# Performance work log

Hardware: AMD Instinct MI355X
Metric: run time of the kernel (lower is better)

Reference implementation:

```python
import jax, jax.numpy as jnp
import numpy as np

N_HEADS, N_LEVELS, N_POINTS, D_MODEL = 8, 3, 12, 64
PARAM_NAMES = ['vp0_w','vp0_b','vp1_w','vp1_b','so0_w','so0_b','so1_w','so1_b','so2_w','so2_b','so3_w','so3_b','aw0_w','aw0_b','aw1_w','aw1_b','aw2_w','aw2_b','aw3_w','aw3_b','op0_w','op0_b','op1_w','op1_b']

def _lrelu(x):
    return jnp.where(x >= 0, x, 0.1 * x)

def _conv(x, w, b):
    y = jax.lax.conv_general_dilated(x, w, (1, 1), 'SAME', dimension_numbers=('NCHW', 'OIHW', 'NCHW'))
    return y + b[None, :, None, None]

def _bilinear(img, px, py):
    # img [B,C,H,W]; px,py [B,Q] absolute pixel coords; zero padding (grid_sample 'zeros')
    B, C, H, W = img.shape
    flat = img.reshape(B, C, H * W)
    x0 = jnp.floor(px); y0 = jnp.floor(py)
    wx1 = px - x0; wy1 = py - y0
    def g(xi, yi, wgt):
        valid = (xi >= 0) & (xi <= W - 1) & (yi >= 0) & (yi <= H - 1)
        xi_c = jnp.clip(xi, 0, W - 1).astype(jnp.int32)
        yi_c = jnp.clip(yi, 0, H - 1).astype(jnp.int32)
        v = jnp.take_along_axis(flat, (yi_c * W + xi_c)[:, None, :], axis=2)
        return v * (wgt * valid)[:, None, :]
    return (g(x0, y0, (1 - wx1) * (1 - wy1)) + g(x0 + 1, y0, wx1 * (1 - wy1))
          + g(x0, y0 + 1, (1 - wx1) * wy1) + g(x0 + 1, y0 + 1, wx1 * wy1))

def _flow_warp(img, flow):
    # img [n,C,h,w]; flow [n,2,h,w] (x,y); matches grid_sample align_corners=True
    n, C, h, w = img.shape
    gy, gx = jnp.meshgrid(jnp.arange(h, dtype=img.dtype), jnp.arange(w, dtype=img.dtype), indexing='ij')
    px = (gx[None] + flow[:, 0]).reshape(n, h * w)
    py = (gy[None] + flow[:, 1]).reshape(n, h * w)
    return _bilinear(img, px, py).reshape(n, C, h, w)

def _forward(x, flow_1, flow_2, flip_flow_1, flip_flow_2, p):
    n, t, c, h, w = x.shape
    hw = h * w; THW = t * hw
    M, L, P, D = N_HEADS, N_LEVELS, N_POINTS, c // N_HEADS
    flow_cn1 = flow_1
    flow_cn2 = flow_1 + _flow_warp(flow_2, flow_1)
    flow_n1c, flow_n1n2 = flip_flow_1, flow_2
    flow_n2n1 = flip_flow_2
    flow_n2c = flip_flow_2 + _flow_warp(flip_flow_1, flip_flow_2)
    warp_cn1 = _flow_warp(x[:, 1], flow_cn1)
    warp_cn2 = _flow_warp(x[:, 2], flow_cn2)
    warp_n1c = _flow_warp(x[:, 0], flow_n1c)
    warp_n1n2 = _flow_warp(x[:, 2], flow_n1n2)
    warp_n2n1 = _flow_warp(x[:, 1], flow_n2n1)
    warp_n2c = _flow_warp(x[:, 0], flow_n2c)
    extra = jnp.concatenate([x[:, 0], warp_cn1, warp_cn2, warp_n1c, warp_n1n2, warp_n2n1, warp_n2c,
                             flow_cn1, flow_cn2, flow_n1c, flow_n1n2, flow_n2n1, flow_n2c], axis=1)
    value = _conv(_lrelu(_conv(x.reshape(n, t * c, h, w), p['vp0_w'], p['vp0_b'])), p['vp1_w'], p['vp1_b'])
    def head(e, pre):
        y = _lrelu(_conv(e, p[pre + '0_w'], p[pre + '0_b']))
        y = _lrelu(_conv(y, p[pre + '1_w'], p[pre + '1_b']))
        y = _lrelu(_conv(y, p[pre + '2_w'], p[pre + '2_b']))
        return _conv(y, p[pre + '3_w'], p[pre + '3_b'])
    so = head(extra, 'so')  # [n, L*M*L*P*2, h, w]
    aw = head(extra, 'aw')  # [n, L*M*L*P*9, h, w]
    so = so.reshape(n, t, -1, hw).transpose(0, 1, 3, 2).reshape(n, THW, M, L, P, 2)
    aw = aw.reshape(n, t, -1, hw).transpose(0, 1, 3, 2).reshape(n, THW, M, L * P * 9)
    aw = jax.nn.softmax(aw, axis=-1).reshape(n, THW, M, L, P * 9)
    # flow-guided offsets: add per-(query-frame, target-level) flow to learned offsets
    off = so.reshape(n, t, hw, M, L, P, 2)
    fz = jnp.zeros_like(flow_cn2)
    def lvl(f0, f1, f2):
        s = jnp.stack([f0, f1, f2], 1)  # [n,3,2,h,w]
        return s.transpose(0, 3, 4, 1, 2).reshape(n, hw, L, 2)[:, None, :, None, :, None, :]
    off = jnp.concatenate([
        off[:, 0:1] + lvl(fz, flow_cn1, flow_cn2),
        off[:, 1:2] + lvl(flow_n1c, fz, flow_n1n2),
        off[:, 2:3] + lvl(flow_n2c, flow_n2n1, fz)], axis=1).reshape(n, THW, M, L, P, 2)
    # 3x3 integer patch around each sampling point
    pi, pj = jnp.meshgrid(jnp.arange(-1, 2), jnp.arange(-1, 2), indexing='ij')
    patch = jnp.stack([pi, pj], -1).reshape(1, 1, 1, 1, 1, 9, 2).astype(off.dtype)
    off = (off[..., None, :] + patch).reshape(n, THW, M, L, P * 9, 2)
    # reference points (valid_ratios are all 1: full masks are zeros)
    ry, rx = jnp.meshgrid((jnp.arange(h) + 0.5) / h, (jnp.arange(w) + 0.5) / w, indexing='ij')
    ref = jnp.stack([rx, ry], -1).reshape(1, hw, 2).astype(off.dtype)
    ref = jnp.tile(ref, (1, t, 1))  # [1, THW, 2]
    norm = jnp.array([w, h], dtype=off.dtype)
    loc = ref[:, :, None, None, None, :] + off / norm  # [n,THW,M,L,P*9,2] normalized
    # multi-scale deformable attention (all L levels share (h,w)); align_corners=False, zeros pad
    P9 = P * 9
    v = value.reshape(n, t, c, hw).transpose(0, 1, 3, 2).reshape(n, THW, M, D)
    vl = v.reshape(n, L, hw, M, D).transpose(0, 3, 1, 4, 2).reshape(n * M * L, D, h, w)
    px = (loc[..., 0] * w - 0.5).transpose(0, 2, 3, 1, 4).reshape(n * M * L, THW * P9)
    py = (loc[..., 1] * h - 0.5).transpose(0, 2, 3, 1, 4).reshape(n * M * L, THW * P9)
    sampled = _bilinear(vl, px, py).reshape(n, M, L, D, THW, P9)
    out = jnp.einsum('nmldqp,nqmlp->nqmd', sampled, aw).reshape(n, THW, c)
    out = out.reshape(n, t, h, w, c).transpose(0, 1, 4, 2, 3).reshape(n, t * c, h, w)
    out = _conv(_lrelu(_conv(out, p['op0_w'], p['op0_b'])), p['op1_w'], p['op1_b'])
    return out.reshape(n, t, c, h, w) + x

def setup_inputs():
    key = jax.random.key(0)
    n, t, c, h, w = 1, 3, 64, 32, 32
    ks = jax.random.split(key, 24)
    d = {}
    d['x'] = jax.random.normal(ks[0], (n, t, c, h, w), jnp.float32)
    for i, name in enumerate(['flow_1', 'flow_2', 'flip_flow_1', 'flip_flow_2']):
        d[name] = jax.random.normal(ks[1 + i], (n, 2, h, w), jnp.float32)
    cin_extra = 7 * c + 12
    specs = [('vp0', t * c, t * c), ('vp1', t * c, t * c),
             ('so0', c, cin_extra), ('so1', c, c), ('so2', c, c), ('so3', N_LEVELS * N_HEADS * N_LEVELS * N_POINTS * 2, c),
             ('aw0', c, cin_extra), ('aw1', c, c), ('aw2', c, c), ('aw3', N_LEVELS * N_HEADS * N_LEVELS * N_POINTS * 9, c),
             ('op0', t * c, t * c), ('op1', t * c, t * c)]
    for i, (name, co, ci) in enumerate(specs):
        kw, kb = jax.random.split(ks[5 + i])
        std = (2.0 / (ci * 9)) ** 0.5
        d[name + '_w'] = jax.random.normal(kw, (co, ci, 3, 3), jnp.float32) * std
        d[name + '_b'] = jax.random.normal(kb, (co,), jnp.float32) * 0.01
    return d

def reference(x, flow_1, flow_2, flip_flow_1, flip_flow_2, vp0_w, vp0_b, vp1_w, vp1_b, so0_w, so0_b, so1_w, so1_b, so2_w, so2_b, so3_w, so3_b, aw0_w, aw0_b, aw1_w, aw1_b, aw2_w, aw2_b, aw3_w, aw3_b, op0_w, op0_b, op1_w, op1_b):
    p = dict(zip(PARAM_NAMES, (vp0_w, vp0_b, vp1_w, vp1_b, so0_w, so0_b, so1_w, so1_b, so2_w, so2_b, so3_w, so3_b, aw0_w, aw0_b, aw1_w, aw1_b, aw2_w, aw2_b, aw3_w, aw3_b, op0_w, op0_b, op1_w, op1_b)))
    return _forward(x, flow_1, flow_2, flip_flow_1, flip_flow_2, p)
```

## Files before the change

kernel.cpp:

```cpp
#include <hip/hip_runtime.h>
#include <math.h>

#define HW 1024

typedef __attribute__((ext_vector_type(8))) short bf16x8;
typedef __attribute__((ext_vector_type(4))) float floatx4;

__device__ __forceinline__ unsigned short f2bf(float f) {
    unsigned u = __float_as_uint(f);
    u += 0x7FFF + ((u >> 16) & 1);
    return (unsigned short)(u >> 16);
}
__device__ __forceinline__ float bf2f(unsigned short u) {
    return __uint_as_float(((unsigned)u) << 16);
}
__device__ __forceinline__ float bflo(unsigned u) { return __uint_as_float(u << 16); }
__device__ __forceinline__ float bfhi(unsigned u) { return __uint_as_float(u & 0xffff0000u); }

template<int CTRL, int RM>
__device__ __forceinline__ float dpp_sum_step(float v) {
    int t = __builtin_amdgcn_update_dpp(0, __float_as_int(v), CTRL, RM, 0xf, true);
    return v + __int_as_float(t);
}
template<int CTRL, int RM>
__device__ __forceinline__ float dpp_max_step(float v) {
    int t = __builtin_amdgcn_update_dpp(__float_as_int(v), __float_as_int(v), CTRL, RM, 0xf, false);
    return fmaxf(v, __int_as_float(t));
}
__device__ __forceinline__ float wave_sum64(float x) {
    x = dpp_sum_step<0x111, 0xf>(x);
    x = dpp_sum_step<0x112, 0xf>(x);
    x = dpp_sum_step<0x114, 0xf>(x);
    x = dpp_sum_step<0x118, 0xf>(x);
    x = dpp_sum_step<0x142, 0xa>(x);
    x = dpp_sum_step<0x143, 0xc>(x);
    return x;
}
__device__ __forceinline__ float wave_max64(float x) {
    x = dpp_max_step<0x111, 0xf>(x);
    x = dpp_max_step<0x112, 0xf>(x);
    x = dpp_max_step<0x114, 0xf>(x);
    x = dpp_max_step<0x118, 0xf>(x);
    x = dpp_max_step<0x142, 0xa>(x);
    x = dpp_max_step<0x143, 0xc>(x);
    return x;
}
__device__ __forceinline__ float bcast_lane63(float x) {
    return __int_as_float(__builtin_amdgcn_readlane(__float_as_int(x), 63));
}

__device__ __forceinline__ float bilin32(const float* __restrict__ img, float px, float py) {
    float x0f = floorf(px), y0f = floorf(py);
    float wx = px - x0f, wy = py - y0f;
    bool vx0 = (x0f >= 0.f) && (x0f <= 31.f);
    bool vx1 = (x0f >= -1.f) && (x0f <= 30.f);
    bool vy0 = (y0f >= 0.f) && (y0f <= 31.f);
    bool vy1 = (y0f >= -1.f) && (y0f <= 30.f);
    int ix0 = (int)fminf(fmaxf(x0f, 0.f), 31.f);
    int iy0 = (int)fminf(fmaxf(y0f, 0.f), 31.f);
    int ix1 = (int)fminf(fmaxf(x0f + 1.f, 0.f), 31.f);
    int iy1 = (int)fminf(fmaxf(y0f + 1.f, 0.f), 31.f);
    float w00 = (1.f - wx) * (1.f - wy) * ((vx0 && vy0) ? 1.f : 0.f);
    float w01 = wx * (1.f - wy) * ((vx1 && vy0) ? 1.f : 0.f);
    float w10 = (1.f - wx) * wy * ((vx0 && vy1) ? 1.f : 0.f);
    float w11 = wx * wy * ((vx1 && vy1) ? 1.f : 0.f);
    return w00 * img[iy0 * 32 + ix0] + w01 * img[iy0 * 32 + ix1] +
           w10 * img[iy1 * 32 + ix0] + w11 * img[iy1 * 32 + ix1];
}

__device__ __forceinline__ float2 comp_flow(const float* __restrict__ fa,
                                            const float* __restrict__ fb, int pix) {
    int y = pix >> 5, x = pix & 31;
    float fx = fa[pix], fy = fa[HW + pix];
    float px = (float)x + fx, py = (float)y + fy;
    float2 r;
    r.x = fx + bilin32(fb, px, py);
    r.y = fy + bilin32(fb + HW, px, py);
    return r;
}

struct WD { const float* src; int cout, Cin, nCb, wbase, beg; };
struct PrepP {
    const float *x, *f1, *f2, *ff1, *ff2;
    float *fcn2, *fn2c;
    unsigned short *x_pad, *extra_pad, *wgt;
    WD wd[12];
};

__global__ __launch_bounds__(256) void prep_k(PrepP P) {
    __shared__ float wlds[16 * 288];
    const int b = blockIdx.x, tid = threadIdx.x;
    if (b < 192) {
        int idx = b * 256 + tid;
        int pix = idx / 48, c4 = idx - pix * 48;
        int y = pix >> 5, xx = pix & 31;
        int c0 = c4 * 4;
        ushort4 s;
        s.x = f2bf(P.x[(size_t)(c0 + 0) * HW + pix]);
        s.y = f2bf(P.x[(size_t)(c0 + 1) * HW + pix]);
        s.z = f2bf(P.x[(size_t)(c0 + 2) * HW + pix]);
        s.w = f2bf(P.x[(size_t)(c0 + 3) * HW + pix]);
        *(ushort4*)(&P.x_pad[(size_t)((y + 1) * 34 + xx + 1) * 192 + c0]) = s;
    } else if (b < 672) {
        int idx = (b - 192) * 256 + tid;
        int pix = idx / 120, c4 = idx - pix * 120;
        int y = pix >> 5, xx = pix & 31;
        int c0 = c4 * 4;
        float va[4];
        if (c0 < 64) {
#pragma unroll
            for (int k = 0; k < 4; ++k) va[k] = P.x[(size_t)(c0 + k) * HW + pix];
        } else if (c0 < 448) {
            int grp = (c0 - 64) >> 6;
            int c = (c0 - 64) & 63;
            const float* src; float fx, fy;
            if (grp == 0)      { src = P.x + 64 * HW;  fx = P.f1[pix];  fy = P.f1[HW + pix]; }
            else if (grp == 1) { src = P.x + 128 * HW; float2 r = comp_flow(P.f1, P.f2, pix);  fx = r.x; fy = r.y; }
            else if (grp == 2) { src = P.x;            fx = P.ff1[pix]; fy = P.ff1[HW + pix]; }
            else if (grp == 3) { src = P.x + 128 * HW; fx = P.f2[pix];  fy = P.f2[HW + pix]; }
            else if (grp == 4) { src = P.x + 64 * HW;  fx = P.ff2[pix]; fy = P.ff2[HW + pix]; }
            else               { src = P.x;            float2 r = comp_flow(P.ff2, P.ff1, pix); fx = r.x; fy = r.y; }
            float px = (float)xx + fx, py = (float)y + fy;
            float x0f = floorf(px), y0f = floorf(py);
            float wx = px - x0f, wy = py - y0f;
            bool vx0 = (x0f >= 0.f) && (x0f <= 31.f);
            bool vx1 = (x0f >= -1.f) && (x0f <= 30.f);
            bool vy0 = (y0f >= 0.f) && (y0f <= 31.f);
            bool vy1 = (y0f >= -1.f) && (y0f <= 30.f);
            int ix0 = (int)fminf(fmaxf(x0f, 0.f), 31.f);
            int iy0 = (int)fminf(fmaxf(y0f, 0.f), 31.f);
            int ix1 = (int)fminf(fmaxf(x0f + 1.f, 0.f), 31.f);
            int iy1 = (int)fminf(fmaxf(y0f + 1.f, 0.f), 31.f);
            float w00 = (1.f - wx) * (1.f - wy) * ((vx0 && vy0) ? 1.f : 0.f);
            float w01 = wx * (1.f - wy) * ((vx1 && vy0) ? 1.f : 0.f);
            float w10 = (1.f - wx) * wy * ((vx0 && vy1) ? 1.f : 0.f);
            float w11 = wx * wy * ((vx1 && vy1) ? 1.f : 0.f);
            int p00 = iy0 * 32 + ix0, p01 = iy0 * 32 + ix1;
            int p10 = iy1 * 32 + ix0, p11 = iy1 * 32 + ix1;
            const float* im = src + (size_t)c * HW;
#pragma unroll
            for (int k = 0; k < 4; ++k) {
                va[k] = w00 * im[p00] + w01 * im[p01] + w10 * im[p10] + w11 * im[p11];
                im += HW;
            }
        } else {
#pragma unroll
            for (int k = 0; k < 4; ++k) {
                int ch = c0 + k;
                float v = 0.f;
                if (ch < 460) {
                    int fc = ch - 448;
                    int which = fc >> 1, comp = fc & 1;
                    if (which == 0)      v = P.f1[comp * HW + pix];
                    else if (which == 1) { float2 r = comp_flow(P.f1, P.f2, pix);  v = comp ? r.y : r.x; }
                    else if (which == 2) v = P.ff1[comp * HW + pix];
                    else if (which == 3) v = P.f2[comp * HW + pix];
                    else if (which == 4) v = P.ff2[comp * HW + pix];
                    else                 { float2 r = comp_flow(P.ff2, P.ff1, pix); v = comp ? r.y : r.x; }
                }
                va[k] = v;
            }
        }
        ushort4 s;
        s.x = f2bf(va[0]); s.y = f2bf(va[1]); s.z = f2bf(va[2]); s.w = f2bf(va[3]);
        *(ushort4*)(&P.extra_pad[(size_t)((y + 1) * 34 + xx + 1) * 480 + c0]) = s;
    } else if (b < 688) {
        int idx = (b - 672) * 256 + tid;
        if (idx < 1024) {
            float2 r = comp_flow(P.f1, P.f2, idx);
            P.fcn2[idx] = r.x; P.fcn2[HW + idx] = r.y;
        } else if (idx < 2048) {
            int pix = idx - 1024;
            float2 r = comp_flow(P.ff2, P.ff1, pix);
            P.fn2c[pix] = r.x; P.fn2c[HW + pix] = r.y;
        }
    } else if (b < 704) {
        const int chans[9] = {192, 192, 480, 64, 64, 64, 64, 192, 192};
        size_t offs[9]; size_t a = 0;
        for (int i = 0; i < 9; ++i) { offs[i] = a; a += (size_t)1156 * chans[i]; }
        int bb = b - 688;
        for (int item = bb; item < 9 * 132; item += 16) {
            int buf = item / 132, i = item - buf * 132;
            int py, px;
            if (i < 34) { py = 0; px = i; }
            else if (i < 68) { py = 33; px = i - 34; }
            else { int j = i - 68; py = 1 + (j >> 1); px = (j & 1) ? 33 : 0; }
            int C = chans[buf];
            unsigned short* p = P.x_pad + offs[buf] + (size_t)(py * 34 + px) * C;
            for (int c = tid; c < C; c += 256) p[c] = 0;
        }
    } else {
        int blk = b - 704;
        int di = 0;
        while (di < 11 && blk >= P.wd[di + 1].beg) ++di;
        WD w = P.wd[di];
        int local = blk - w.beg;
        int co16 = local / w.nCb, cb = local - co16 * w.nCb;
        int cr0 = co16 * 16, ci0 = cb * 32;
        for (int i = tid; i < 16 * 288; i += 256) {
            int cr = i / 288, o = i - cr * 288;
            int crg = cr0 + cr, ci = ci0 + o / 9;
            float v = (crg < w.cout && ci < w.Cin)
                ? w.src[((size_t)crg * w.Cin + ci0) * 9 + o] : 0.f;
            wlds[i] = v;
        }
        __syncthreads();
        for (int e = tid; e < 9 * 512; e += 256) {
            int t = e >> 9, idx = e & 511;
            int j = idx & 7, lane = idx >> 3, q = lane >> 4, mm = lane & 15;
            P.wgt[((size_t)w.wbase + ((size_t)co16 * 9 + t) * w.nCb + cb) * 512 + idx] =
                f2bf(wlds[mm * 288 + (q * 8 + j) * 9 + t]);
        }
    }
}

struct CDesc {
    const unsigned short* in;
    const unsigned short* wgt;
    const float* bias;
    void* out;
    const float* residual;
    int Cpad, nCb, Cout, mode, cmod, relu, Mblocks;
};
struct CParam { CDesc d[4]; };

template<int PIXROWS, int COBLK>
__global__ __launch_bounds__(256) void conv_mfma_k(CParam P) {
    constexpr int TROWS = PIXROWS + 2;
    constexpr int TC = TROWS * 34 * 4;
    constexpr int ITRIPS = (TC + 255) / 256;
    constexpr int NTY = PIXROWS / 4;
    constexpr int NACC = NTY * 2;
    constexpr int MT = COBLK / 16;
    constexpr int WN = MT * 9 * 64;
    constexpr int WTRIPS = (WN + 255) / 256;
    __shared__ unsigned short blds[TROWS * 34 * 40];
    __shared__ unsigned short wlds[MT * 9 * 512];

    int bx = blockIdx.x;
    int di = 0;
    while (bx >= P.d[di].Mblocks) { bx -= P.d[di].Mblocks; ++di; }
    const CDesc d = P.d[di];

    const int tid = threadIdx.x;
    const int w = tid >> 6, lane = tid & 63;
    const int lq = lane >> 4, ln = lane & 15;
    const int co0 = bx * COBLK;
    const int by = blockIdx.y, y0 = by * PIXROWS;
    const unsigned short* __restrict__ in = d.in;
    const unsigned short* __restrict__ wg = d.wgt;
    const int Cpad = d.Cpad, nCb = d.nCb;

    floatx4 acc[MT][NACC];
#pragma unroll
    for (int mt = 0; mt < MT; ++mt)
#pragma unroll
        for (int nt = 0; nt < NACC; ++nt)
            acc[mt][nt] = (floatx4){0.f, 0.f, 0.f, 0.f};

    bf16x8 ireg[ITRIPS];
    bf16x8 wreg[WTRIPS];

    auto load_regs = [&](int cb) {
        const int ci0 = cb << 5;
#pragma unroll
        for (int k = 0; k < ITRIPS; ++k) {
            int i = tid + k * 256;
            if (i < TC) {
                int r = i / 136, rem = i - r * 136, c = rem >> 2, g = rem & 3;
                ireg[k] = *(const bf16x8*)(in + (size_t)((y0 + r) * 34 + c) * Cpad + ci0 + g * 8);
            }
        }
#pragma unroll
        for (int k = 0; k < WTRIPS; ++k) {
            int i = tid + k * 256;
            if (i < WN) {
                int chunk = i >> 6, l16 = i & 63;
                int mt = chunk / 9, t = chunk - mt * 9;
                wreg[k] = *(const bf16x8*)(wg + ((size_t)(((co0 >> 4) + mt) * 9 + t) * nCb + cb) * 512 + l16 * 8);
            }
        }
    };

    load_regs(0);

    for (int cb = 0; cb < nCb; ++cb) {
        __syncthreads();
#pragma unroll
        for (int k = 0; k < ITRIPS; ++k) {
            int i = tid + k * 256;
            if (i < TC) {
                int r = i / 136, rem = i - r * 136, c = rem >> 2, g = rem & 3;
                *(bf16x8*)(&blds[(r * 34 + c) * 40 + g * 8]) = ireg[k];
            }
        }
#pragma unroll
        for (int k = 0; k < WTRIPS; ++k) {
            int i = tid + k * 256;
            if (i < WN) {
                int chunk = i >> 6, l16 = i & 63;
                *(bf16x8*)(&wlds[chunk * 512 + l16 * 8]) = wreg[k];
            }
        }
        __syncthreads();
        if (cb + 1 < nCb) load_regs(cb + 1);
        for (int t = 0; t < 9; ++t) {
            const int dy = t / 3, dx = t - dy * 3;
            bf16x8 bfr[NACC];
#pragma unroll
            for (int ty = 0; ty < NTY; ++ty)
#pragma unroll
                for (int tx = 0; tx < 2; ++tx) {
                    int yy = w * NTY + ty + dy;
                    int xx = tx * 16 + ln + dx;
                    bfr[ty * 2 + tx] = *(const bf16x8*)(&blds[(yy * 34 + xx) * 40 + lq * 8]);
                }
#pragma unroll
            for (int mt = 0; mt < MT; ++mt) {
                bf16x8 afr = *(const bf16x8*)(&wlds[(mt * 9 + t) * 512 + lane * 8]);
#pragma unroll
                for (int nt = 0; nt < NACC; ++nt)
                    acc[mt][nt] = __builtin_amdgcn_mfma_f32_16x16x32_bf16(afr, bfr[nt], acc[mt][nt], 0, 0, 0);
            }
        }
    }

#pragma unroll
    for (int mt = 0; mt < MT; ++mt) {
        const int co = co0 + mt * 16 + lq * 4;
        if (co >= d.Cout) continue;
        float bv[4];
#pragma unroll
        for (int r = 0; r < 4; ++r) bv[r] = d.bias[co + r];
#pragma unroll
        for (int nt = 0; nt < NACC; ++nt) {
            const int ty = nt >> 1, tx = nt & 1;
            const int pix = by * (PIXROWS * 32) + (w * NTY + ty) * 32 + tx * 16 + ln;
            float v[4];
#pragma unroll
            for (int r = 0; r < 4; ++r) {
                float vv = acc[mt][nt][r] + bv[r];
                if (d.relu) vv = (vv >= 0.f) ? vv : 0.1f * vv;
                v[r] = vv;
            }
            if (d.mode == 0) {
                float* o = (float*)d.out;
#pragma unroll
                for (int r = 0; r < 4; ++r) {
                    float vv = v[r];
                    if (d.residual) vv += d.residual[(size_t)(co + r) * HW + pix];
                    o[(size_t)(co + r) * HW + pix] = vv;
                }
            } else if (d.mode == 1) {
                int fq = co / d.cmod, cc = co - fq * d.cmod;
                *(float4*)((float*)d.out + ((size_t)fq * HW + pix) * d.cmod + cc) =
                    make_float4(v[0], v[1], v[2], v[3]);
            } else if (d.mode == 2) {
                int fq = co / d.cmod, cc = co - fq * d.cmod;
                ushort4 s4;
                s4.x = f2bf(v[0]); s4.y = f2bf(v[1]); s4.z = f2bf(v[2]); s4.w = f2bf(v[3]);
                *(ushort4*)((unsigned short*)d.out + ((size_t)fq * HW + pix) * d.cmod + cc) = s4;
            } else {
                int yy = (pix >> 5) + 1, xx = (pix & 31) + 1;
                ushort4 s4;
                s4.x = f2bf(v[0]); s4.y = f2bf(v[1]); s4.z = f2bf(v[2]); s4.w = f2bf(v[3]);
                *(ushort4*)((unsigned short*)d.out + (size_t)(yy * 34 + xx) * d.cmod + co) = s4;
            }
        }
    }
}

struct L4Desc {
    const unsigned short* in;
    const unsigned short* wgt;
    const float* bias;
    void* out;
    int mode, cmod, Mblocks;
};
struct L4Param { L4Desc d[2]; };

__global__ __launch_bounds__(256) void conv_l4_k(L4Param P) {
    __shared__ unsigned short blds[10 * 34 * 40];
    __shared__ unsigned short wlds[9 * 2 * 512];

    int bx = blockIdx.x;
    int di = 0;
    if (bx >= P.d[0].Mblocks) { bx -= P.d[0].Mblocks; di = 1; }
    const L4Desc d = P.d[di];

    const int tid = threadIdx.x;
    const int w = tid >> 6, lane = tid & 63;
    const int lq = lane >> 4, ln = lane & 15;
    const int co0 = bx * 16;
    const unsigned short* __restrict__ in = d.in;
    const unsigned short* __restrict__ wg = d.wgt;

    bf16x8 wreg[5];
#pragma unroll
    for (int k = 0; k < 5; ++k) {
        int i = tid + k * 256;
        if (i < 1152) {
            int chunk = i >> 6, l16 = i & 63;
            int t = chunk >> 1, cb = chunk & 1;
            wreg[k] = *(const bf16x8*)(wg + (((size_t)bx * 9 + t) * 2 + cb) * 512 + l16 * 8);
        }
    }

    bf16x8 ireg[6];
    auto load_in = [&](int y0, int cb) {
        const int ci0 = cb << 5;
#pragma unroll
        for (int k = 0; k < 6; ++k) {
            int i = tid + k * 256;
            if (i < 1360) {
                int r = i / 136, rem = i - r * 136, c = rem >> 2, g = rem & 3;
                ireg[k] = *(const bf16x8*)(in + (size_t)((y0 + r) * 34 + c) * 64 + ci0 + g * 8);
            }
        }
    };
    load_in(0, 0);

#pragma unroll
    for (int k = 0; k < 5; ++k) {
        int i = tid + k * 256;
        if (i < 1152) *(bf16x8*)(&wlds[(i >> 6) * 512 + (i & 63) * 8]) = wreg[k];
    }

    floatx4 acc[4];
#pragma unroll
    for (int nt = 0; nt < 4; ++nt) acc[nt] = (floatx4){0.f, 0.f, 0.f, 0.f};

    for (int p = 0; p < 8; ++p) {
        const int y = p >> 1, cb = p & 1;
        __syncthreads();
#pragma unroll
        for (int k = 0; k < 6; ++k) {
            int i = tid + k * 256;
            if (i < 1360) {
                int r = i / 136, rem = i - r * 136, c = rem >> 2, g = rem & 3;
                *(bf16x8*)(&blds[(r * 34 + c) * 40 + g * 8]) = ireg[k];
            }
        }
        __syncthreads();
        if (p < 7) { int pn = p + 1; load_in((pn >> 1) * 8, pn & 1); }
#pragma unroll
        for (int t = 0; t < 9; ++t) {
            const int dy = t / 3, dx = t - dy * 3;
            bf16x8 afr = *(const bf16x8*)(&wlds[(t * 2 + cb) * 512 + lane * 8]);
#pragma unroll
            for (int ty = 0; ty < 2; ++ty)
#pragma unroll
                for (int tx = 0; tx < 2; ++tx) {
                    int yy = w * 2 + ty + dy;
                    int xx = tx * 16 + ln + dx;
                    bf16x8 bfr = *(const bf16x8*)(&blds[(yy * 34 + xx) * 40 + lq * 8]);
                    acc[ty * 2 + tx] =
                        __builtin_amdgcn_mfma_f32_16x16x32_bf16(afr, bfr, acc[ty * 2 + tx], 0, 0, 0);
                }
        }
        if (cb == 1) {
            const int co = co0 + lq * 4;
            float bv[4];
#pragma unroll
            for (int r2 = 0; r2 < 4; ++r2) bv[r2] = d.bias[co + r2];
            int fq = co / d.cmod, cc = co - fq * d.cmod;
#pragma unroll
            for (int nt = 0; nt < 4; ++nt) {
                const int ty = nt >> 1, tx = nt & 1;
                const int pix = y * 256 + (w * 2 + ty) * 32 + tx * 16 + ln;
                float v0 = acc[nt][0] + bv[0], v1 = acc[nt][1] + bv[1];
                float v2 = acc[nt][2] + bv[2], v3 = acc[nt][3] + bv[3];
                if (d.mode == 1) {
                    *(float4*)((float*)d.out + ((size_t)fq * HW + pix) * d.cmod + cc) =
                        make_float4(v0, v1, v2, v3);
                } else {
                    ushort4 s4;
                    s4.x = f2bf(v0); s4.y = f2bf(v1); s4.z = f2bf(v2); s4.w = f2bf(v3);
                    *(ushort4*)((unsigned short*)d.out + ((size_t)fq * HW + pix) * d.cmod + cc) = s4;
                }
                acc[nt] = (floatx4){0.f, 0.f, 0.f, 0.f};
            }
        }
    }
}

__global__ __launch_bounds__(256) void deform_attn_k(
    const unsigned short* __restrict__ value_b, const float* __restrict__ so_t,
    const unsigned short* __restrict__ aw_t,
    const float* __restrict__ flow_1, const float* __restrict__ flow_2,
    const float* __restrict__ flip_flow_1, const float* __restrict__ flip_flow_2,
    const float* __restrict__ flow_cn2, const float* __restrict__ flow_n2c,
    unsigned short* __restrict__ attn_pad)
{
    __shared__ unsigned short pwlds[4][432];
    const int tid = threadIdx.x;
    const int wav = tid >> 6, lane = tid & 63;
    const int m = blockIdx.x & 7, qc = blockIdx.x >> 3;

    const int pp = lane & 15, gq = lane >> 4;
    const int gdy = (gq >> 1) * 2 - 1;
    const int gdx = (gq & 1) * 2 - 1;
    const bool selx = (gq & 1);
    const bool sely = (gq >> 1);

    const unsigned short* __restrict__ vm = value_b + (size_t)m * 8192;

    for (int r = 0; r < 8; ++r) {
        const int q = qc * 32 + r * 4 + wav;
        const int f = q >> 10, pix = q & 1023;
        const int y = pix >> 5, x = pix & 31;

        float av[6];
        {
            const unsigned short* awp = aw_t + (size_t)q * 2592 + m * 324;
#pragma unroll
            for (int it = 0; it < 6; ++it) {
                int j = lane + it * 64;
                av[it] = (j < 324) ? bf2f(awp[j]) : -1e30f;
            }
        }

        float vmax = -1e30f;
#pragma unroll
        for (int it = 0; it < 6; ++it) vmax = fmaxf(vmax, av[it]);
        vmax = bcast_lane63(wave_max64(vmax));
        float ssum = 0.f;
#pragma unroll
        for (int it = 0; it < 6; ++it) {
            int j = lane + it * 64;
            float e = (j < 324) ? __expf(av[it] - vmax) : 0.f;
            av[it] = e;
            ssum += e;
        }
        ssum = bcast_lane63(wave_sum64(ssum));
        const float inv = 1.f / ssum;

#pragma unroll
        for (int it = 0; it < 6; ++it) {
            int j = lane + it * 64;
            if (j < 324) {
                int pi = j / 9, k = j - pi * 9;
                pwlds[wav][pi * 12 + k] = f2bf(av[it] * inv);
            }
        }

        const float* sop = so_t + (size_t)q * 576 + m * 72;
        float2 so2r[3];
#pragma unroll
        for (int pt = 0; pt < 3; ++pt) {
            int pi = pt * 16 + pp;
            if (pi < 36) so2r[pt] = *(const float2*)(sop + pi * 2);
            else { so2r[pt].x = 0.f; so2r[pt].y = 0.f; }
        }

        float flx0 = 0.f, fly0 = 0.f, flx1 = 0.f, fly1 = 0.f, flx2 = 0.f, fly2 = 0.f;
        if (f == 0) {
            flx1 = flow_1[pix];      fly1 = flow_1[HW + pix];
            flx2 = flow_cn2[pix];    fly2 = flow_cn2[HW + pix];
        } else if (f == 1) {
            flx0 = flip_flow_1[pix]; fly0 = flip_flow_1[HW + pix];
            flx2 = flow_2[pix];      fly2 = flow_2[HW + pix];
        } else {
            flx0 = flow_n2c[pix];    fly0 = flow_n2c[HW + pix];
            flx1 = flip_flow_2[pix]; fly1 = flip_flow_2[HW + pix];
        }

        float acc[8];
#pragma unroll
        for (int dd = 0; dd < 8; ++dd) acc[dd] = 0.f;

#pragma unroll
        for (int pt = 0; pt < 3; ++pt) {
            int pi = pt * 16 + pp;
            if (pi < 36) {
                int l = pi / 12;
                float2 so2 = so2r[pt];
                float fx = (l == 0) ? flx0 : (l == 1) ? flx1 : flx2;
                float fy = (l == 0) ? fly0 : (l == 1) ? fly1 : fly2;
                float bxf = (float)x + so2.x + fx;
                float byf = (float)y + so2.y + fy;
                float x0f = floorf(bxf), y0f = floorf(byf);
                float wx = bxf - x0f, wy = byf - y0f;
                float ax = 1.f - wx, ay = 1.f - wy;
                int x0 = (int)fminf(fmaxf(x0f, -2.f), 34.f);
                int y0 = (int)fminf(fmaxf(y0f, -2.f), 34.f);

                const unsigned short* pr = &pwlds[wav][pi * 12];
                uint2 pv0 = *(const uint2*)(pr);
                uint2 pv1 = *(const uint2*)(pr + 4);
                float a0 = bflo(pv0.x), a1 = bfhi(pv0.x), a2 = bflo(pv0.y);
                float a3 = bfhi(pv0.y), a4 = bflo(pv1.x), a5 = bfhi(pv1.x);
                float a6 = bflo(pv1.y), a7 = bfhi(pv1.y), a8 = bf2f(pr[8]);

                float bs0a, bs0b, bs1a, bs1b, bs2a, bs2b;
                {
                    float b0, b1, b2, b3;
                    b0 = a0 * ax; b1 = a0 * wx + a3 * ax; b2 = a3 * wx + a6 * ax; b3 = a6 * wx;
                    bs0a = selx ? b2 : b0; bs0b = selx ? b3 : b1;
                    b0 = a1 * ax; b1 = a1 * wx + a4 * ax; b2 = a4 * wx + a7 * ax; b3 = a7 * wx;
                    bs1a = selx ? b2 : b0; bs1b = selx ? b3 : b1;
                    b0 = a2 * ax; b1 = a2 * wx + a5 * ax; b2 = a5 * wx + a8 * ax; b3 = a8 * wx;
                    bs2a = selx ? b2 : b0; bs2b = selx ? b3 : b1;
                }
                float c00, c01, c10, c11;
                {
                    float c0 = bs0a * ay, c1 = bs0a * wy + bs1a * ay;
                    float c2 = bs1a * wy + bs2a * ay, c3 = bs2a * wy;
                    c00 = sely ? c2 : c0; c10 = sely ? c3 : c1;
                    c0 = bs0b * ay; c1 = bs0b * wy + bs1b * ay;
                    c2 = bs1b * wy + bs2b * ay; c3 = bs2b * wy;
                    c01 = sely ? c2 : c0; c11 = sely ? c3 : c1;
                }
                float cg[2][2] = {{c00, c01}, {c10, c11}};
                const unsigned short* __restrict__ vl = vm + (size_t)l * 65536;
#pragma unroll
                for (int sy = 0; sy < 2; ++sy) {
#pragma unroll
                    for (int sx = 0; sx < 2; ++sx) {
                        int dy = gdy + sy, dx = gdx + sx;
                        float pyf = y0f + (float)dy, pxf = x0f + (float)dx;
                        bool v = (pxf >= 0.f) && (pxf <= 31.f) && (pyf >= 0.f) && (pyf <= 31.f);
                        int px = min(max(x0 + dx, 0), 31);
                        int py = min(max(y0 + dy, 0), 31);
                        float c = cg[sy][sx] * (v ? 1.f : 0.f);
                        uint4 vv = *(const uint4*)(vl + (size_t)(py * 32 + px) * 8);
                        acc[0] = fmaf(c, bflo(vv.x), acc[0]);
                        acc[1] = fmaf(c, bfhi(vv.x), acc[1]);
                        acc[2] = fmaf(c, bflo(vv.y), acc[2]);
                        acc[3] = fmaf(c, bfhi(vv.y), acc[3]);
                        acc[4] = fmaf(c, bflo(vv.z), acc[4]);
                        acc[5] = fmaf(c, bfhi(vv.z), acc[5]);
                        acc[6] = fmaf(c, bflo(vv.w), acc[6]);
                        acc[7] = fmaf(c, bfhi(vv.w), acc[7]);
                    }
                }
            }
        }

#pragma unroll
        for (int dd = 0; dd < 8; ++dd) acc[dd] = wave_sum64(acc[dd]);
        if (lane == 63) {
            unsigned short* op = attn_pad + (size_t)((y + 1) * 34 + x + 1) * 192 + f * 64 + m * 8;
            ushort4 s0, s1;
            s0.x = f2bf(acc[0]); s0.y = f2bf(acc[1]); s0.z = f2bf(acc[2]); s0.w = f2bf(acc[3]);
            s1.x = f2bf(acc[4]); s1.y = f2bf(acc[5]); s1.z = f2bf(acc[6]); s1.w = f2bf(acc[7]);
            *(ushort4*)(op) = s0;
            *(ushort4*)(op + 4) = s1;
        }
    }
}

extern "C" void kernel_launch(void* const* d_in, const int* in_sizes, int n_in,
                              void* d_out, int out_size, void* d_ws, size_t ws_size,
                              hipStream_t stream) {
    const float* x      = (const float*)d_in[0];
    const float* flow_1 = (const float*)d_in[1];
    const float* flow_2 = (const float*)d_in[2];
    const float* flip_1 = (const float*)d_in[3];
    const float* flip_2 = (const float*)d_in[4];
    const float* vp0_w = (const float*)d_in[5];  const float* vp0_b = (const float*)d_in[6];
    const float* vp1_w = (const float*)d_in[7];  const float* vp1_b = (const float*)d_in[8];
    const float* so0_w = (const float*)d_in[9];  const float* so0_b = (const float*)d_in[10];
    const float* so1_w = (const float*)d_in[11]; const float* so1_b = (const float*)d_in[12];
    const float* so2_w = (const float*)d_in[13]; const float* so2_b = (const float*)d_in[14];
    const float* so3_w = (const float*)d_in[15]; const float* so3_b = (const float*)d_in[16];
    const float* aw0_w = (const float*)d_in[17]; const float* aw0_b = (const float*)d_in[18];
    const float* aw1_w = (const float*)d_in[19]; const float* aw1_b = (const float*)d_in[20];
    const float* aw2_w = (const float*)d_in[21]; const float* aw2_b = (const float*)d_in[22];
    const float* aw3_w = (const float*)d_in[23]; const float* aw3_b = (const float*)d_in[24];
    const float* op0_w = (const float*)d_in[25]; const float* op0_b = (const float*)d_in[26];
    const float* op1_w = (const float*)d_in[27]; const float* op1_b = (const float*)d_in[28];
    float* out = (float*)d_out;
    (void)ws_size; (void)in_sizes; (void)n_in; (void)out_size;

    float* fws = (float*)d_ws;
    float* flow_cn2 = fws;
    float* flow_n2c = flow_cn2 + 2048;
    unsigned short* value_b = (unsigned short*)(flow_n2c + 2048);
    float* so_t     = (float*)(value_b + 196608);
    unsigned short* uws = (unsigned short*)(so_t + 1769472);
    unsigned short* x_pad     = uws;
    unsigned short* vp0h      = x_pad + 1156 * 192;
    unsigned short* extra_pad = vp0h + 1156 * 192;
    unsigned short* s1 = extra_pad + 1156 * 480;
    unsigned short* a1 = s1 + 1156 * 64;
    unsigned short* s2 = a1 + 1156 * 64;
    unsigned short* a2 = s2 + 1156 * 64;
    unsigned short* attn_pad = a2 + 1156 * 64;
    unsigned short* op0h     = attn_pad + 1156 * 192;
    unsigned short* aw_t = op0h + 1156 * 192;
    unsigned short* wgt  = aw_t + (size_t)3072 * 2592;

    PrepP pp;
    pp.x = x; pp.f1 = flow_1; pp.f2 = flow_2; pp.ff1 = flip_1; pp.ff2 = flip_2;
    pp.fcn2 = flow_cn2; pp.fn2c = flow_n2c;
    pp.x_pad = x_pad; pp.extra_pad = extra_pad; pp.wgt = wgt;
    pp.wd[0]  = {vp0_w, 192, 192, 6,     0,    0};
    pp.wd[1]  = {vp1_w, 192, 192, 6,   648,   72};
    pp.wd[2]  = {so0_w,  64, 460, 15, 1296,  144};
    pp.wd[3]  = {aw0_w,  64, 460, 15, 1836,  204};
    pp.wd[4]  = {so1_w,  64,  64, 2,  2376,  264};
    pp.wd[5]  = {aw1_w,  64,  64, 2,  2448,  272};
    pp.wd[6]  = {so2_w,  64,  64, 2,  2520,  280};
    pp.wd[7]  = {aw2_w,  64,  64, 2,  2592,  288};
    pp.wd[8]  = {so3_w, 1728, 64, 2,  2664,  296};
    pp.wd[9]  = {aw3_w, 7776, 64, 2,  4608,  512};
    pp.wd[10] = {op0_w, 192, 192, 6, 13392, 1488};
    pp.wd[11] = {op1_w, 192, 192, 6, 14040, 1560};
    prep_k<<<2336, 256, 0, stream>>>(pp);

    const int BIG = 1 << 30;
    CDesc nul = {nullptr, nullptr, nullptr, nullptr, nullptr, 0, 0, 0, 0, 0, 0, BIG};

    {
        CParam cp;
        cp.d[0] = {x_pad,     wgt + (size_t)0 * 512,    vp0_b, vp0h, nullptr, 192, 6,  192, 3, 192, 1, 12};
        cp.d[1] = {extra_pad, wgt + (size_t)1296 * 512, so0_b, s1,   nullptr, 480, 15, 64,  3, 64,  1, 4};
        cp.d[2] = {extra_pad, wgt + (size_t)1836 * 512, aw0_b, a1,   nullptr, 480, 15, 64,  3, 64,  1, 4};
        cp.d[3] = nul;
        conv_mfma_k<4, 16><<<dim3(20, 8), 256, 0, stream>>>(cp);
    }
    {
        CParam cp;
        cp.d[0] = {vp0h, wgt + (size_t)648 * 512,  vp1_b, value_b, nullptr, 192, 6, 192, 2, 8,  0, 12};
        cp.d[1] = {s1,   wgt + (size_t)2376 * 512, so1_b, s2,      nullptr, 64,  2, 64,  3, 64, 1, 4};
        cp.d[2] = {a1,   wgt + (size_t)2448 * 512, aw1_b, a2,      nullptr, 64,  2, 64,  3, 64, 1, 4};
        cp.d[3] = nul;
        conv_mfma_k<4, 16><<<dim3(20, 8), 256, 0, stream>>>(cp);
    }
    {
        CParam cp;
        cp.d[0] = {s2, wgt + (size_t)2520 * 512, so2_b, s1, nullptr, 64, 2, 64, 3, 64, 1, 4};
        cp.d[1] = {a2, wgt + (size_t)2592 * 512, aw2_b, a1, nullptr, 64, 2, 64, 3, 64, 1, 4};
        cp.d[2] = nul; cp.d[3] = nul;
        conv_mfma_k<4, 16><<<dim3(8, 8), 256, 0, stream>>>(cp);
    }
    {
        L4Param lp;
        lp.d[0] = {s1, wgt + (size_t)2664 * 512, so3_b, so_t, 1, 576,  108};
        lp.d[1] = {a1, wgt + (size_t)4608 * 512, aw3_b, aw_t, 2, 2592, 486};
        conv_l4_k<<<594, 256, 0, stream>>>(lp);
    }

    deform_attn_k<<<768, 256, 0, stream>>>(value_b, so_t, aw_t,
                                           flow_1, flow_2, flip_1, flip_2,
                                           flow_cn2, flow_n2c, attn_pad);

    {
        CParam cp;
        cp.d[0] = {attn_pad, wgt + (size_t)13392 * 512, op0_b, op0h, nullptr, 192, 6, 192, 3, 192, 1, 12};
        cp.d[1] = nul; cp.d[2] = nul; cp.d[3] = nul;
        conv_mfma_k<4, 16><<<dim3(12, 8), 256, 0, stream>>>(cp);
    }
    {
        CParam cp;
        cp.d[0] = {op0h, wgt + (size_t)14040 * 512, op1_b, out, x, 192, 6, 192, 0, 0, 0, 12};
        cp.d[1] = nul; cp.d[2] = nul; cp.d[3] = nul;
        conv_mfma_k<4, 16><<<dim3(12, 8), 256, 0, stream>>>(cp);
    }
}
```

Baseline: 260.2 us.

## Fuse post-prep conv, deform and output stages into persistent megakernel with grid barriers

Replaces seven separate kernel launches (three conv layers, the L4 conv, deformable attention, two output convs) with one persistent kernel that loops over each phase's work items and separates phases with a software grid-wide atomic barrier. The barrier counters are reset inside prep_k. The aim is to remove per-launch overhead and inter-kernel gaps. In exchange, the grid is capped at the occupancy-derived number of co-resident blocks, so phases with more items than blocks run them serially. A single shared-memory buffer is reused across phases, which may lower occupancy, and the spin barrier relies on all blocks being co-resident.

```diff
diff --git a/kernel.cpp b/kernel.cpp
--- a/kernel.cpp
+++ b/kernel.cpp
@@ -47,6 +47,25 @@
 }
 __device__ __forceinline__ float bcast_lane63(float x) {
     return __int_as_float(__builtin_amdgcn_readlane(__float_as_int(x), 63));
+}
+
+__device__ __forceinline__ void gbar(unsigned* bar, unsigned nblk) {
+    __syncthreads();
+    if (threadIdx.x == 0) {
+        __threadfence();
+        unsigned g = __hip_atomic_load(bar + 1, __ATOMIC_ACQUIRE, __HIP_MEMORY_SCOPE_AGENT);
+        unsigned a = __hip_atomic_fetch_add(bar, 1u, __ATOMIC_ACQ_REL, __HIP_MEMORY_SCOPE_AGENT);
+        if (a == nblk - 1u) {
+            __hip_atomic_store(bar, 0u, __ATOMIC_RELAXED, __HIP_MEMORY_SCOPE_AGENT);
+            __hip_atomic_fetch_add(bar + 1, 1u, __ATOMIC_ACQ_REL, __HIP_MEMORY_SCOPE_AGENT);
+        } else {
+            while (__hip_atomic_load(bar + 1, __ATOMIC_ACQUIRE, __HIP_MEMORY_SCOPE_AGENT) == g) {
+                __builtin_amdgcn_s_sleep(4);
+            }
+        }
+        __threadfence();
+    }
+    __syncthreads();
 }
 
 __device__ __forceinline__ float bilin32(const float* __restrict__ img, float px, float py) {
@@ -84,6 +103,7 @@
     const float *x, *f1, *f2, *ff1, *ff2;
     float *fcn2, *fn2c;
     unsigned short *x_pad, *extra_pad, *wgt;
+    unsigned* bar;
     WD wd[12];
 };
 
@@ -166,6 +186,7 @@
         *(ushort4*)(&P.extra_pad[(size_t)((y + 1) * 34 + xx + 1) * 480 + c0]) = s;
     } else if (b < 688) {
         int idx = (b - 672) * 256 + tid;
+        if (b == 672 && tid == 0) { P.bar[0] = 0u; P.bar[1] = 0u; }
         if (idx < 1024) {
             float2 r = comp_flow(P.f1, P.f2, idx);
             P.fcn2[idx] = r.x; P.fcn2[HW + idx] = r.y;
@@ -223,30 +244,30 @@
     int Cpad, nCb, Cout, mode, cmod, relu, Mblocks;
 };
 struct CParam { CDesc d[4]; };
-
-template<int PIXROWS, int COBLK>
-__global__ __launch_bounds__(256) void conv_mfma_k(CParam P) {
-    constexpr int TROWS = PIXROWS + 2;
-    constexpr int TC = TROWS * 34 * 4;
-    constexpr int ITRIPS = (TC + 255) / 256;
-    constexpr int NTY = PIXROWS / 4;
-    constexpr int NACC = NTY * 2;
-    constexpr int MT = COBLK / 16;
-    constexpr int WN = MT * 9 * 64;
-    constexpr int WTRIPS = (WN + 255) / 256;
-    __shared__ unsigned short blds[TROWS * 34 * 40];
-    __shared__ unsigned short wlds[MT * 9 * 512];
-
-    int bx = blockIdx.x;
+struct L4Desc {
+    const unsigned short* in;
+    const unsigned short* wgt;
+    const float* bias;
+    void* out;
+    int mode, cmod, Mblocks;
+};
+struct L4Param { L4Desc d[2]; };
+
+__device__ void conv_phase(const CParam& P, int item, int NX, int tid,
+                           unsigned short* blds, unsigned short* wlds) {
+    constexpr int TROWS = 6, TC = TROWS * 34 * 4, ITRIPS = 4;
+    constexpr int NTY = 1, NACC = 2, MT = 1, WN = 576, WTRIPS = 3;
+
+    int bx = item % NX;
+    const int by = item / NX;
     int di = 0;
     while (bx >= P.d[di].Mblocks) { bx -= P.d[di].Mblocks; ++di; }
     const CDesc d = P.d[di];
 
-    const int tid = threadIdx.x;
     const int w = tid >> 6, lane = tid & 63;
     const int lq = lane >> 4, ln = lane & 15;
-    const int co0 = bx * COBLK;
-    const int by = blockIdx.y, y0 = by * PIXROWS;
+    const int co0 = bx * 16;
+    const int y0 = by * 4;
     const unsigned short* __restrict__ in = d.in;
     const unsigned short* __restrict__ wg = d.wgt;
     const int Cpad = d.Cpad, nCb = d.nCb;
@@ -335,7 +356,7 @@
 #pragma unroll
         for (int nt = 0; nt < NACC; ++nt) {
             const int ty = nt >> 1, tx = nt & 1;
-            const int pix = by * (PIXROWS * 32) + (w * NTY + ty) * 32 + tx * 16 + ln;
+            const int pix = by * 128 + (w * NTY + ty) * 32 + tx * 16 + ln;
             float v[4];
 #pragma unroll
             for (int r = 0; r < 4; ++r) {
@@ -370,25 +391,14 @@
     }
 }
 
-struct L4Desc {
-    const unsigned short* in;
-    const unsigned short* wgt;
-    const float* bias;
-    void* out;
-    int mode, cmod, Mblocks;
-};
-struct L4Param { L4Desc d[2]; };
-
-__global__ __launch_bounds__(256) void conv_l4_k(L4Param P) {
-    __shared__ unsigned short blds[10 * 34 * 40];
-    __shared__ unsigned short wlds[9 * 2 * 512];
-
-    int bx = blockIdx.x;
+__device__ void l4_phase(const L4Param& P, int item, int tid,
+                         unsigned short* blds, unsigned short* wlds) {
+    __syncthreads();
+    int bx = item;
     int di = 0;
     if (bx >= P.d[0].Mblocks) { bx -= P.d[0].Mblocks; di = 1; }
     const L4Desc d = P.d[di];
 
-    const int tid = threadIdx.x;
     const int w = tid >> 6, lane = tid & 63;
     const int lq = lane >> 4, ln = lane & 15;
     const int co0 = bx * 16;
@@ -484,18 +494,21 @@
     }
 }
 
-__global__ __launch_bounds__(256) void deform_attn_k(
-    const unsigned short* __restrict__ value_b, const float* __restrict__ so_t,
-    const unsigned short* __restrict__ aw_t,
-    const float* __restrict__ flow_1, const float* __restrict__ flow_2,
-    const float* __restrict__ flip_flow_1, const float* __restrict__ flip_flow_2,
-    const float* __restrict__ flow_cn2, const float* __restrict__ flow_n2c,
-    unsigned short* __restrict__ attn_pad)
-{
-    __shared__ unsigned short pwlds[4][432];
-    const int tid = threadIdx.x;
+struct MegaP {
+    CParam l1, l2, l3, opa, opb;
+    L4Param l4;
+    const unsigned short* value_b;
+    const float* so_t;
+    const unsigned short* aw_t;
+    const float *f1, *f2, *ff1, *ff2, *fcn2, *fn2c;
+    unsigned short* attn_pad;
+    unsigned* bar;
+};
+
+__device__ void deform_phase(const MegaP& M, int item, int tid,
+                             unsigned short (*pwlds)[432]) {
     const int wav = tid >> 6, lane = tid & 63;
-    const int m = blockIdx.x & 7, qc = blockIdx.x >> 3;
+    const int m = item & 7, qc = item >> 3;
 
     const int pp = lane & 15, gq = lane >> 4;
     const int gdy = (gq >> 1) * 2 - 1;
@@ -503,7 +516,7 @@
     const bool selx = (gq & 1);
     const bool sely = (gq >> 1);
 
-    const unsigned short* __restrict__ vm = value_b + (size_t)m * 8192;
+    const unsigned short* __restrict__ vm = M.value_b + (size_t)m * 8192;
 
     for (int r = 0; r < 8; ++r) {
         const int q = qc * 32 + r * 4 + wav;
@@ -512,7 +525,7 @@
 
         float av[6];
         {
-            const unsigned short* awp = aw_t + (size_t)q * 2592 + m * 324;
+            const unsigned short* awp = M.aw_t + (size_t)q * 2592 + m * 324;
 #pragma unroll
             for (int it = 0; it < 6; ++it) {
                 int j = lane + it * 64;
@@ -544,7 +557,7 @@
             }
         }
 
-        const float* sop = so_t + (size_t)q * 576 + m * 72;
+        const float* sop = M.so_t + (size_t)q * 576 + m * 72;
         float2 so2r[3];
 #pragma unroll
         for (int pt = 0; pt < 3; ++pt) {
@@ -555,14 +568,14 @@
 
         float flx0 = 0.f, fly0 = 0.f, flx1 = 0.f, fly1 = 0.f, flx2 = 0.f, fly2 = 0.f;
         if (f == 0) {
-            flx1 = flow_1[pix];      fly1 = flow_1[HW + pix];
-            flx2 = flow_cn2[pix];    fly2 = flow_cn2[HW + pix];
+            flx1 = M.f1[pix];   fly1 = M.f1[HW + pix];
+            flx2 = M.fcn2[pix]; fly2 = M.fcn2[HW + pix];
         } else if (f == 1) {
-            flx0 = flip_flow_1[pix]; fly0 = flip_flow_1[HW + pix];
-            flx2 = flow_2[pix];      fly2 = flow_2[HW + pix];
+            flx0 = M.ff1[pix];  fly0 = M.ff1[HW + pix];
+            flx2 = M.f2[pix];   fly2 = M.f2[HW + pix];
         } else {
-            flx0 = flow_n2c[pix];    fly0 = flow_n2c[HW + pix];
-            flx1 = flip_flow_2[pix]; fly1 = flip_flow_2[HW + pix];
+            flx0 = M.fn2c[pix]; fly0 = M.fn2c[HW + pix];
+            flx1 = M.ff2[pix];  fly1 = M.ff2[HW + pix];
         }
 
         float acc[8];
@@ -640,7 +653,7 @@
 #pragma unroll
         for (int dd = 0; dd < 8; ++dd) acc[dd] = wave_sum64(acc[dd]);
         if (lane == 63) {
-            unsigned short* op = attn_pad + (size_t)((y + 1) * 34 + x + 1) * 192 + f * 64 + m * 8;
+            unsigned short* op = M.attn_pad + (size_t)((y + 1) * 34 + x + 1) * 192 + f * 64 + m * 8;
             ushort4 s0, s1;
             s0.x = f2bf(acc[0]); s0.y = f2bf(acc[1]); s0.z = f2bf(acc[2]); s0.w = f2bf(acc[3]);
             s1.x = f2bf(acc[4]); s1.y = f2bf(acc[5]); s1.z = f2bf(acc[6]); s1.w = f2bf(acc[7]);
@@ -648,6 +661,27 @@
             *(ushort4*)(op + 4) = s1;
         }
     }
+}
+
+__global__ __launch_bounds__(256) void mega_k(MegaP M) {
+    __shared__ unsigned short SMEM[22816];
+    const int tid = threadIdx.x;
+    const unsigned nb = gridDim.x;
+
+    for (int it = blockIdx.x; it < 160; it += nb) conv_phase(M.l1, it, 20, tid, SMEM, SMEM + 8160);
+    gbar(M.bar, nb);
+    for (int it = blockIdx.x; it < 160; it += nb) conv_phase(M.l2, it, 20, tid, SMEM, SMEM + 8160);
+    gbar(M.bar, nb);
+    for (int it = blockIdx.x; it < 64;  it += nb) conv_phase(M.l3, it, 8,  tid, SMEM, SMEM + 8160);
+    gbar(M.bar, nb);
+    for (int it = blockIdx.x; it < 594; it += nb) l4_phase(M.l4, it, tid, SMEM, SMEM + 13600);
+    gbar(M.bar, nb);
+    for (int it = blockIdx.x; it < 768; it += nb)
+        deform_phase(M, it, tid, reinterpret_cast<unsigned short(*)[432]>(SMEM));
+    gbar(M.bar, nb);
+    for (int it = blockIdx.x; it < 96;  it += nb) conv_phase(M.opa, it, 12, tid, SMEM, SMEM + 8160);
+    gbar(M.bar, nb);
+    for (int it = blockIdx.x; it < 96;  it += nb) conv_phase(M.opb, it, 12, tid, SMEM, SMEM + 8160);
 }
 
 extern "C" void kernel_launch(void* const* d_in, const int* in_sizes, int n_in,
@@ -690,11 +724,12 @@
     unsigned short* op0h     = attn_pad + 1156 * 192;
     unsigned short* aw_t = op0h + 1156 * 192;
     unsigned short* wgt  = aw_t + (size_t)3072 * 2592;
+    unsigned* bar = (unsigned*)(wgt + (size_t)14688 * 512);
 
     PrepP pp;
     pp.x = x; pp.f1 = flow_1; pp.f2 = flow_2; pp.ff1 = flip_1; pp.ff2 = flip_2;
     pp.fcn2 = flow_cn2; pp.fn2c = flow_n2c;
-    pp.x_pad = x_pad; pp.extra_pad = extra_pad; pp.wgt = wgt;
+    pp.x_pad = x_pad; pp.extra_pad = extra_pad; pp.wgt = wgt; pp.bar = bar;
     pp.wd[0]  = {vp0_w, 192, 192, 6,     0,    0};
     pp.wd[1]  = {vp1_w, 192, 192, 6,   648,   72};
     pp.wd[2]  = {so0_w,  64, 460, 15, 1296,  144};
@@ -712,50 +747,33 @@
     const int BIG = 1 << 30;
     CDesc nul = {nullptr, nullptr, nullptr, nullptr, nullptr, 0, 0, 0, 0, 0, 0, BIG};
 
-    {
-        CParam cp;
-        cp.d[0] = {x_pad,     wgt + (size_t)0 * 512,    vp0_b, vp0h, nullptr, 192, 6,  192, 3, 192, 1, 12};
-        cp.d[1] = {extra_pad, wgt + (size_t)1296 * 512, so0_b, s1,   nullptr, 480, 15, 64,  3, 64,  1, 4};
-        cp.d[2] = {extra_pad, wgt + (size_t)1836 * 512, aw0_b, a1,   nullptr, 480, 15, 64,  3, 64,  1, 4};
-        cp.d[3] = nul;
-        conv_mfma_k<4, 16><<<dim3(20, 8), 256, 0, stream>>>(cp);
-    }
-    {
-        CParam cp;
-        cp.d[0] = {vp0h, wgt + (size_t)648 * 512,  vp1_b, value_b, nullptr, 192, 6, 192, 2, 8,  0, 12};
-        cp.d[1] = {s1,   wgt + (size_t)2376 * 512, so1_b, s2,      nullptr, 64,  2, 64,  3, 64, 1, 4};
-        cp.d[2] = {a1,   wgt + (size_t)2448 * 512, aw1_b, a2,      nullptr, 64,  2, 64,  3, 64, 1, 4};
-        cp.d[3] = nul;
-        conv_mfma_k<4, 16><<<dim3(20, 8), 256, 0, stream>>>(cp);
-    }
-    {
-        CParam cp;
-        cp.d[0] = {s2, wgt + (size_t)2520 * 512, so2_b, s1, nullptr, 64, 2, 64, 3, 64, 1, 4};
-        cp.d[1] = {a2, wgt + (size_t)2592 * 512, aw2_b, a1, nullptr, 64, 2, 64, 3, 64, 1, 4};
-        cp.d[2] = nul; cp.d[3] = nul;
-        conv_mfma_k<4, 16><<<dim3(8, 8), 256, 0, stream>>>(cp);
-    }
-    {
-        L4Param lp;
-        lp.d[0] = {s1, wgt + (size_t)2664 * 512, so3_b, so_t, 1, 576,  108};
-        lp.d[1] = {a1, wgt + (size_t)4608 * 512, aw3_b, aw_t, 2, 2592, 486};
-        conv_l4_k<<<594, 256, 0, stream>>>(lp);
-    }
-
-    deform_attn_k<<<768, 256, 0, stream>>>(value_b, so_t, aw_t,
-                                           flow_1, flow_2, flip_1, flip_2,
-                                           flow_cn2, flow_n2c, attn_pad);
-
-    {
-        CParam cp;
-        cp.d[0] = {attn_pad, wgt + (size_t)13392 * 512, op0_b, op0h, nullptr, 192, 6, 192, 3, 192, 1, 12};
-        cp.d[1] = nul; cp.d[2] = nul; cp.d[3] = nul;
-        conv_mfma_k<4, 16><<<dim3(12, 8), 256, 0, stream>>>(cp);
-    }
-    {
-        CParam cp;
-        cp.d[0] = {op0h, wgt + (size_t)14040 * 512, op1_b, out, x, 192, 6, 192, 0, 0, 0, 12};
-        cp.d[1] = nul; cp.d[2] = nul; cp.d[3] = nul;
-        conv_mfma_k<4, 16><<<dim3(12, 8), 256, 0, stream>>>(cp);
-    }
-}
+    MegaP M;
+    M.l1.d[0] = {x_pad,     wgt + (size_t)0 * 512,    vp0_b, vp0h, nullptr, 192, 6,  192, 3, 192, 1, 12};
+    M.l1.d[1] = {extra_pad, wgt + (size_t)1296 * 512, so0_b, s1,   nullptr, 480, 15, 64,  3, 64,  1, 4};
+    M.l1.d[2] = {extra_pad, wgt + (size_t)1836 * 512, aw0_b, a1,   nullptr, 480, 15, 64,  3, 64,  1, 4};
+    M.l1.d[3] = nul;
+    M.l2.d[0] = {vp0h, wgt + (size_t)648 * 512,  vp1_b, value_b, nullptr, 192, 6, 192, 2, 8,  0, 12};
+    M.l2.d[1] = {s1,   wgt + (size_t)2376 * 512, so1_b, s2,      nullptr, 64,  2, 64,  3, 64, 1, 4};
+    M.l2.d[2] = {a1,   wgt + (size_t)2448 * 512, aw1_b, a2,      nullptr, 64,  2, 64,  3, 64, 1, 4};
+    M.l2.d[3] = nul;
+    M.l3.d[0] = {s2, wgt + (size_t)2520 * 512, so2_b, s1, nullptr, 64, 2, 64, 3, 64, 1, 4};
+    M.l3.d[1] = {a2, wgt + (size_t)2592 * 512, aw2_b, a1, nullptr, 64, 2, 64, 3, 64, 1, 4};
+    M.l3.d[2] = nul; M.l3.d[3] = nul;
+    M.l4.d[0] = {s1, wgt + (size_t)2664 * 512, so3_b, so_t, 1, 576,  108};
+    M.l4.d[1] = {a1, wgt + (size_t)4608 * 512, aw3_b, aw_t, 2, 2592, 486};
+    M.opa.d[0] = {attn_pad, wgt + (size_t)13392 * 512, op0_b, op0h, nullptr, 192, 6, 192, 3, 192, 1, 12};
+    M.opa.d[1] = nul; M.opa.d[2] = nul; M.opa.d[3] = nul;
+    M.opb.d[0] = {op0h, wgt + (size_t)14040 * 512, op1_b, out, x, 192, 6, 192, 0, 0, 0, 12};
+    M.opb.d[1] = nul; M.opb.d[2] = nul; M.opb.d[3] = nul;
+    M.value_b = value_b; M.so_t = so_t; M.aw_t = aw_t;
+    M.f1 = flow_1; M.f2 = flow_2; M.ff1 = flip_1; M.ff2 = flip_2;
+    M.fcn2 = flow_cn2; M.fn2c = flow_n2c;
+    M.attn_pad = attn_pad; M.bar = bar;
+
+    int maxb = 0;
+    if (hipOccupancyMaxActiveBlocksPerMultiprocessor(&maxb, mega_k, 256, 0) != hipSuccess || maxb < 1)
+        maxb = 1;
+    if (maxb > 3) maxb = 3;
+    int grid = maxb * 256;
+    mega_k<<<grid, 256, 0, stream>>>(M);
+}
```

Result: slower. 736.7 us (+183.1%).
